# Kernel tuning notes

Measured on AMD Instinct MI355X. Metric: run time of the kernel, lower is better.

Reference implementation:

```python
import jax, jax.numpy as jnp
import numpy as np

EMSIZE = 1024
NHEAD = 16
HEAD = EMSIZE // NHEAD


def setup_inputs() -> dict:
    key = jax.random.key(0)
    ks = jax.random.split(key, 8)
    s = 1.0 / np.sqrt(EMSIZE)
    return {
        "embed": jax.random.normal(ks[0], (2, 2048, EMSIZE), dtype=jnp.float32),
        "q": jax.random.normal(ks[1], (2, 2048, EMSIZE), dtype=jnp.float32),
        "Wk": jax.random.normal(ks[2], (EMSIZE, EMSIZE), dtype=jnp.float32) * s,
        "bk": jnp.zeros((EMSIZE,), dtype=jnp.float32),
        "Wq": jax.random.normal(ks[3], (EMSIZE, EMSIZE), dtype=jnp.float32) * s,
        "bq": jnp.zeros((EMSIZE,), dtype=jnp.float32),
        "Wv": jax.random.normal(ks[4], (EMSIZE, EMSIZE), dtype=jnp.float32) * s,
        "bv": jnp.zeros((EMSIZE,), dtype=jnp.float32),
    }


def _split_heads(x):
    # [b, s, E] -> [b, h, s, d]
    b, s, _ = x.shape
    return x.reshape(b, s, NHEAD, HEAD).transpose(0, 2, 1, 3)


def reference(embed, q, Wk, bk, Wq, bq, Wv, bv):
    # torch Linear: y = x @ W.T + b
    k = _split_heads(embed @ Wk.T + bk)   # [b, h, skv, d]
    qh = _split_heads(q @ Wq.T + bq)      # [b, h, sq, d]
    v = _split_heads(embed @ Wv.T + bv)   # [b, h, skv, d]
    scale = 1.0 / np.sqrt(HEAD).astype(np.float32)
    scores = jnp.einsum("bhqd,bhkd->bhqk", qh, k) * scale
    attn = jax.nn.softmax(scores, axis=-1)  # dropout p=0 -> identity
    ctx = jnp.einsum("bhqk,bhkd->bhqd", attn, v)
    b, h, sq, d = ctx.shape
    return ctx.transpose(0, 2, 1, 3).reshape(b, sq, h * d)
```

## Files before the change

kernel.cpp:

```cpp
#include <hip/hip_runtime.h>
#include <cstdint>
#include <cstddef>


using bf16 = __bf16;
typedef __bf16 bf16x8 __attribute__((ext_vector_type(8)));
typedef float f32x4 __attribute__((ext_vector_type(4)));
typedef float f32x16 __attribute__((ext_vector_type(16)));
using uint32 = unsigned int;

__device__ __forceinline__ void async16(void* lds, const void* g) {
  __builtin_amdgcn_global_load_lds((__attribute__((address_space(1))) void*)g,
                                   (__attribute__((address_space(3))) void*)lds,
                                   16, 0, 0);
}

__device__ __forceinline__ uint32 pack_bf16x2(float lo, float hi_) {
  union { bf16 h[2]; uint32 u; } w;
  w.h[0] = (bf16)lo; w.h[1] = (bf16)hi_;
  return w.u;
}

__global__ void cast_all_kernel(const float* __restrict__ e, const float* __restrict__ q,
                                const float* __restrict__ wk, const float* __restrict__ wq,
                                const float* __restrict__ wv, bf16* __restrict__ dst) {
  int i = blockIdx.x * blockDim.x + threadIdx.x;
  if (i >= 2883584) return;
  const float* src; int off;
  if (i < 1048576)      { src = e;  off = 0; }
  else if (i < 2097152) { src = q;  off = 1048576; }
  else if (i < 2359296) { src = wk; off = 2097152; }
  else if (i < 2621440) { src = wq; off = 2359296; }
  else                  { src = wv; off = 2621440; }
  float4 v = reinterpret_cast<const float4*>(src)[i - off];
  union { bf16 h[4]; unsigned long long u; } o;
  o.h[0] = (bf16)v.x; o.h[1] = (bf16)v.y; o.h[2] = (bf16)v.z; o.h[3] = (bf16)v.w;
  reinterpret_cast<unsigned long long*>(dst)[i] = o.u;
}

__global__ __launch_bounds__(256) void proj_kernel(
    const bf16* __restrict__ emb, const bf16* __restrict__ qin,
    const bf16* __restrict__ wk, const bf16* __restrict__ wq, const bf16* __restrict__ wv,
    const float* __restrict__ bk, const float* __restrict__ bq, const float* __restrict__ bv,
    bf16* __restrict__ Kp, bf16* __restrict__ Qp, bf16* __restrict__ Vt)
{
  __shared__ bf16 As[128 * 64];
  __shared__ bf16 Bs[128 * 64];

  int pid = blockIdx.x;
  int proj = pid >> 8;
  int t = pid & 255;
  int m0 = (t >> 3) * 128;
  int n0 = (t & 7) * 128;

  const bf16* A = (proj == 1) ? qin : emb;
  const bf16* W = (proj == 0) ? wk : (proj == 1) ? wq : wv;
  const float* bias = (proj == 0) ? bk : (proj == 1) ? bq : bv;
  const bool proj2 = (proj == 2);

  int tid = threadIdx.x;
  int lane = tid & 63, wid = tid >> 6;
  int quad = lane >> 4, l16 = lane & 15;
  int moff = (wid & 1) * 64, noff = (wid >> 1) * 64;

  f32x4 zero = {0.f, 0.f, 0.f, 0.f};
  f32x4 acc[4][4];
#pragma unroll
  for (int i = 0; i < 4; i++)
#pragma unroll
    for (int j = 0; j < 4; j++) acc[i][j] = zero;

  for (int kk = 0; kk < 1024; kk += 64) {
    __syncthreads();
#pragma unroll
    for (int i = 0; i < 4; i++) {
      int c = i * 256 + tid;
      int row = c >> 3;
      int ko = ((c ^ row) & 7) << 3;
      async16(&As[(size_t)(i * 256 + wid * 64) * 8], &A[(size_t)(m0 + row) * 1024 + kk + ko]);
      async16(&Bs[(size_t)(i * 256 + wid * 64) * 8], &W[(size_t)(n0 + row) * 1024 + kk + ko]);
    }
    __syncthreads();
#pragma unroll
    for (int ks = 0; ks < 2; ks++) {
      bf16x8 af[4], bfr[4];
#pragma unroll
      for (int i = 0; i < 4; i++) {
        int row = moff + i * 16 + l16;
        af[i] = *reinterpret_cast<const bf16x8*>(&As[row * 64 + ((((ks << 2) | quad) ^ row) & 7) * 8]);
      }
#pragma unroll
      for (int j = 0; j < 4; j++) {
        int row = noff + j * 16 + l16;
        bfr[j] = *reinterpret_cast<const bf16x8*>(&Bs[row * 64 + ((((ks << 2) | quad) ^ row) & 7) * 8]);
      }
      if (proj2) {
#pragma unroll
        for (int i = 0; i < 4; i++)
#pragma unroll
          for (int j = 0; j < 4; j++)
            acc[i][j] = __builtin_amdgcn_mfma_f32_16x16x32_bf16(bfr[j], af[i], acc[i][j], 0, 0, 0);
      } else {
#pragma unroll
        for (int i = 0; i < 4; i++)
#pragma unroll
          for (int j = 0; j < 4; j++)
            acc[i][j] = __builtin_amdgcn_mfma_f32_16x16x32_bf16(af[i], bfr[j], acc[i][j], 0, 0, 0);
      }
    }
  }

  if (proj2) {
#pragma unroll
    for (int i = 0; i < 4; i++) {
      int grow = m0 + moff + i * 16 + l16;
      int bb = grow >> 11;
      int ss = grow & 2047;
#pragma unroll
      for (int j = 0; j < 4; j++) {
#pragma unroll
        for (int r = 0; r < 4; r++) {
          int gcol = n0 + noff + j * 16 + quad * 4 + r;
          int hh = gcol >> 6, dd = gcol & 63;
          int bh = bb * 16 + hh;
          float v = acc[i][j][r] + bias[gcol];
          Vt[((size_t)bh * 64 + dd) * 2048 + ss] = (bf16)v;
        }
      }
    }
  } else {
    float bvv[4];
#pragma unroll
    for (int j = 0; j < 4; j++) bvv[j] = bias[n0 + noff + j * 16 + l16];
    bf16* dst = (proj == 0) ? Kp : Qp;
    const float qs = (proj == 1) ? 0.18033688011112042f : 1.0f;
#pragma unroll
    for (int i = 0; i < 4; i++) {
#pragma unroll
      for (int r = 0; r < 4; r++) {
        int grow = m0 + moff + i * 16 + quad * 4 + r;
        int bb = grow >> 11;
        int ss = grow & 2047;
#pragma unroll
        for (int j = 0; j < 4; j++) {
          int gcol = n0 + noff + j * 16 + l16;
          int hh = gcol >> 6, dd = gcol & 63;
          int bh = bb * 16 + hh;
          float v = (acc[i][j][r] + bvv[j]) * qs;
          dst[((size_t)bh * 2048 + ss) * 64 + dd] = (bf16)v;
        }
      }
    }
  }
}

__global__ __launch_bounds__(256, 4) void attn_kernel(
    const bf16* __restrict__ Qp, const bf16* __restrict__ Kp, const bf16* __restrict__ Vt,
    float* __restrict__ out, float* __restrict__ part1, float* __restrict__ lbuf)
{
  __shared__ bf16 Ks[2][64 * 64];
  __shared__ bf16 Vs[2][64 * 64];

  int bid = blockIdx.x;
  int half = bid & 1;
  int q0 = ((bid >> 1) & 15) << 7;
  int bh = bid >> 5;
  int bb = bh >> 4, hh = bh & 15;
  int g0 = half << 4;

  const bf16* Qg = Qp + (size_t)bh * (2048 * 64);
  const bf16* Kg = Kp + (size_t)bh * (2048 * 64);
  const bf16* Vg = Vt + (size_t)bh * (64 * 2048);

  int tid = threadIdx.x, lane = tid & 63, wid = tid >> 6;
  int l32 = lane & 31;
  int h = lane >> 5;
  int wq0 = q0 + wid * 32;

  auto stage = [&](int kt_, int buf) {
#pragma unroll
    for (int i = 0; i < 2; i++) {
      int c = i * 256 + tid;
      int row = c >> 3;
      int srow = (row & ~12) | ((row & 4) << 1) | ((row & 8) >> 1);
      int ko = ((c ^ row) & 7) << 3;
      async16(&Ks[buf][(size_t)(i * 256 + wid * 64) * 8], &Kg[(size_t)(kt_ * 64 + srow) * 64 + ko]);
      async16(&Vs[buf][(size_t)(i * 256 + wid * 64) * 8], &Vg[(size_t)row * 2048 + kt_ * 64 + ko]);
    }
  };

  bf16x8 qf[4];
#pragma unroll
  for (int s = 0; s < 4; s++)
    qf[s] = *reinterpret_cast<const bf16x8*>(
        &Qg[(size_t)(wq0 + l32) * 64 + s * 16 + h * 8]);

  stage(g0, 0);

  const f32x16 z16 = {0.f, 0.f, 0.f, 0.f, 0.f, 0.f, 0.f, 0.f,
                      0.f, 0.f, 0.f, 0.f, 0.f, 0.f, 0.f, 0.f};
  f32x16 Ov[2];
  Ov[0] = z16; Ov[1] = z16;
  float l_i = 0.f;

  for (int kt = 0; kt < 16; kt++) {
    int cur = kt & 1;
    __syncthreads();
    __builtin_amdgcn_sched_barrier(0);
    if (kt < 15) stage(g0 + kt + 1, cur ^ 1);
    __builtin_amdgcn_sched_barrier(0);

    const bf16* Kc = Ks[cur];
    const bf16* Vc = Vs[cur];

    f32x16 St[2];
#pragma unroll
    for (int t = 0; t < 2; t++) {
      int row = t * 32 + l32;
      {
        bf16x8 kf = *reinterpret_cast<const bf16x8*>(&Kc[row * 64 + ((h ^ row) & 7) * 8]);
        St[t] = __builtin_amdgcn_mfma_f32_32x32x16_bf16(kf, qf[0], z16, 0, 0, 0);
      }
#pragma unroll
      for (int s = 1; s < 4; s++) {
        int j8 = s * 2 + h;
        bf16x8 kf = *reinterpret_cast<const bf16x8*>(&Kc[row * 64 + ((j8 ^ row) & 7) * 8]);
        St[t] = __builtin_amdgcn_mfma_f32_32x32x16_bf16(kf, qf[s], St[t], 0, 0, 0);
      }
    }

#pragma unroll
    for (int t = 0; t < 2; t++)
#pragma unroll
      for (int i = 0; i < 16; i++) {
        float p = __builtin_amdgcn_exp2f(St[t][i]);
        St[t][i] = p;
        l_i += p;
      }

#pragma unroll
    for (int t = 0; t < 2; t++)
#pragma unroll
      for (int g = 0; g < 2; g++) {
        union { uint32 u[4]; bf16x8 v; } pb;
#pragma unroll
        for (int i = 0; i < 4; i++)
          pb.u[i] = pack_bf16x2(St[t][g * 8 + 2 * i], St[t][g * 8 + 2 * i + 1]);
        int j8 = t * 4 + g * 2 + h;
#pragma unroll
        for (int dt = 0; dt < 2; dt++) {
          int rowv = dt * 32 + l32;
          bf16x8 vf = *reinterpret_cast<const bf16x8*>(&Vc[rowv * 64 + ((j8 ^ rowv) & 7) * 8]);
          Ov[dt] = __builtin_amdgcn_mfma_f32_32x32x16_bf16(vf, pb.v, Ov[dt], 0, 0, 0);
        }
      }
  }

  float l_tot = l_i + __shfl_xor(l_i, 32);
  int q = wq0 + l32;
  float* dstO = (half == 0 ? out : part1) + ((size_t)bb * 2048 + q) * 1024 + hh * 64;
#pragma unroll
  for (int dt = 0; dt < 2; dt++)
#pragma unroll
    for (int g = 0; g < 4; g++) {
      float4 o;
      o.x = Ov[dt][4 * g + 0];
      o.y = Ov[dt][4 * g + 1];
      o.z = Ov[dt][4 * g + 2];
      o.w = Ov[dt][4 * g + 3];
      *reinterpret_cast<float4*>(&dstO[dt * 32 + g * 8 + 4 * h]) = o;
    }
  if (h == 0) lbuf[half * 65536 + (bh << 11) + q] = l_tot;
}

__global__ __launch_bounds__(256) void combine_kernel(
    float* __restrict__ out, const float* __restrict__ part1,
    const float* __restrict__ lbuf) {
  int i = blockIdx.x * 256 + threadIdx.x;
  int e = i << 2;
  int brow = e >> 10;
  int b = brow >> 11;
  int hcol = (e >> 6) & 15;
  int srow = brow & 2047;
  int lidx = ((b * 16 + hcol) << 11) + srow;
  float inv = 1.0f / (lbuf[lidx] + lbuf[65536 + lidx]);
  float4 a = reinterpret_cast<const float4*>(out)[i];
  float4 p = reinterpret_cast<const float4*>(part1)[i];
  float4 r;
  r.x = (a.x + p.x) * inv;
  r.y = (a.y + p.y) * inv;
  r.z = (a.z + p.z) * inv;
  r.w = (a.w + p.w) * inv;
  reinterpret_cast<float4*>(out)[i] = r;
}

extern "C" void kernel_launch(void* const* d_in, const int* in_sizes, int n_in,
                              void* d_out, int out_size, void* d_ws, size_t ws_size,
                              hipStream_t stream) {
  (void)in_sizes; (void)n_in; (void)out_size; (void)ws_size;
  const float* embed = (const float*)d_in[0];
  const float* qin   = (const float*)d_in[1];
  const float* Wk    = (const float*)d_in[2];
  const float* bk    = (const float*)d_in[3];
  const float* Wq    = (const float*)d_in[4];
  const float* bq    = (const float*)d_in[5];
  const float* Wv    = (const float*)d_in[6];
  const float* bv    = (const float*)d_in[7];
  float* out = (float*)d_out;

  bf16* ws = (bf16*)d_ws;
  bf16* emb_bf = ws;
  bf16* q_bf   = emb_bf + 4194304;
  bf16* wk_bf  = q_bf   + 4194304;
  bf16* wq_bf  = wk_bf  + 1048576;
  bf16* wv_bf  = wq_bf  + 1048576;
  bf16* Kp     = wv_bf  + 1048576;
  bf16* Qp     = Kp     + 4194304;
  bf16* Vt     = Qp     + 4194304;

  float* part1 = (float*)d_ws;
  float* lbuf  = part1 + 4194304;

  cast_all_kernel<<<11264, 256, 0, stream>>>(embed, qin, Wk, Wq, Wv, ws);

  proj_kernel<<<768, 256, 0, stream>>>(emb_bf, q_bf, wk_bf, wq_bf, wv_bf,
                                       bk, bq, bv, Kp, Qp, Vt);
  attn_kernel<<<1024, 256, 0, stream>>>(Qp, Kp, Vt, out, part1, lbuf);
  combine_kernel<<<4096, 256, 0, stream>>>(out, part1, lbuf);
}
```

Before: 194.5 us.

## Generalize attention KV split to four ways when workspace allows

```diff
diff --git a/kernel.cpp b/kernel.cpp
--- a/kernel.cpp
+++ b/kernel.cpp
@@ -154,19 +154,22 @@
   }
 }
 
-__global__ __launch_bounds__(256, 4) void attn_kernel(
+__global__ __launch_bounds__(256, 5) void attn_kernel(
     const bf16* __restrict__ Qp, const bf16* __restrict__ Kp, const bf16* __restrict__ Vt,
-    float* __restrict__ out, float* __restrict__ part1, float* __restrict__ lbuf)
+    float* __restrict__ out, float* __restrict__ part, float* __restrict__ lbuf,
+    int lsplit)
 {
   __shared__ bf16 Ks[2][64 * 64];
   __shared__ bf16 Vs[2][64 * 64];
 
   int bid = blockIdx.x;
-  int half = bid & 1;
-  int q0 = ((bid >> 1) & 15) << 7;
-  int bh = bid >> 5;
+  int nsplit = 1 << lsplit;
+  int half = bid & (nsplit - 1);
+  int q0 = ((bid >> lsplit) & 15) << 7;
+  int bh = bid >> (4 + lsplit);
   int bb = bh >> 4, hh = bh & 15;
-  int g0 = half << 4;
+  int ntiles = 32 >> lsplit;
+  int g0 = half * ntiles;
 
   const bf16* Qg = Qp + (size_t)bh * (2048 * 64);
   const bf16* Kg = Kp + (size_t)bh * (2048 * 64);
@@ -203,11 +206,11 @@
   Ov[0] = z16; Ov[1] = z16;
   float l_i = 0.f;
 
-  for (int kt = 0; kt < 16; kt++) {
+  for (int kt = 0; kt < ntiles; kt++) {
     int cur = kt & 1;
     __syncthreads();
     __builtin_amdgcn_sched_barrier(0);
-    if (kt < 15) stage(g0 + kt + 1, cur ^ 1);
+    if (kt < ntiles - 1) stage(g0 + kt + 1, cur ^ 1);
     __builtin_amdgcn_sched_barrier(0);
 
     const bf16* Kc = Ks[cur];
@@ -258,7 +261,8 @@
 
   float l_tot = l_i + __shfl_xor(l_i, 32);
   int q = wq0 + l32;
-  float* dstO = (half == 0 ? out : part1) + ((size_t)bb * 2048 + q) * 1024 + hh * 64;
+  float* dstO = (half == 0 ? out : part + (size_t)(half - 1) * 4194304)
+                + ((size_t)bb * 2048 + q) * 1024 + hh * 64;
 #pragma unroll
   for (int dt = 0; dt < 2; dt++)
 #pragma unroll
@@ -274,8 +278,8 @@
 }
 
 __global__ __launch_bounds__(256) void combine_kernel(
-    float* __restrict__ out, const float* __restrict__ part1,
-    const float* __restrict__ lbuf) {
+    float* __restrict__ out, const float* __restrict__ part,
+    const float* __restrict__ lbuf, int nsplit) {
   int i = blockIdx.x * 256 + threadIdx.x;
   int e = i << 2;
   int brow = e >> 10;
@@ -283,21 +287,24 @@
   int hcol = (e >> 6) & 15;
   int srow = brow & 2047;
   int lidx = ((b * 16 + hcol) << 11) + srow;
-  float inv = 1.0f / (lbuf[lidx] + lbuf[65536 + lidx]);
+  float lsum = lbuf[lidx];
+#pragma unroll 3
+  for (int s = 1; s < nsplit; s++) lsum += lbuf[s * 65536 + lidx];
   float4 a = reinterpret_cast<const float4*>(out)[i];
-  float4 p = reinterpret_cast<const float4*>(part1)[i];
-  float4 r;
-  r.x = (a.x + p.x) * inv;
-  r.y = (a.y + p.y) * inv;
-  r.z = (a.z + p.z) * inv;
-  r.w = (a.w + p.w) * inv;
-  reinterpret_cast<float4*>(out)[i] = r;
+#pragma unroll 3
+  for (int s = 1; s < nsplit; s++) {
+    float4 p = reinterpret_cast<const float4*>(part)[(size_t)(s - 1) * 1048576 + i];
+    a.x += p.x; a.y += p.y; a.z += p.z; a.w += p.w;
+  }
+  float inv = 1.0f / lsum;
+  a.x *= inv; a.y *= inv; a.z *= inv; a.w *= inv;
+  reinterpret_cast<float4*>(out)[i] = a;
 }
 
 extern "C" void kernel_launch(void* const* d_in, const int* in_sizes, int n_in,
                               void* d_out, int out_size, void* d_ws, size_t ws_size,
                               hipStream_t stream) {
-  (void)in_sizes; (void)n_in; (void)out_size; (void)ws_size;
+  (void)in_sizes; (void)n_in; (void)out_size;
   const float* embed = (const float*)d_in[0];
   const float* qin   = (const float*)d_in[1];
   const float* Wk    = (const float*)d_in[2];
@@ -318,13 +325,21 @@
   bf16* Qp     = Kp     + 4194304;
   bf16* Vt     = Qp     + 4194304;
 
-  float* part1 = (float*)d_ws;
-  float* lbuf  = part1 + 4194304;
+  const bool big = (ws_size >= 99614720ull);
+  const int lsplit = big ? 2 : 1;
+  float* part, *lbuf;
+  if (big) {
+    part = (float*)((char*)d_ws + 48234496);
+    lbuf = part + 3 * 4194304;
+  } else {
+    part = (float*)d_ws;
+    lbuf = part + 4194304;
+  }
 
   cast_all_kernel<<<11264, 256, 0, stream>>>(embed, qin, Wk, Wq, Wv, ws);
 
   proj_kernel<<<768, 256, 0, stream>>>(emb_bf, q_bf, wk_bf, wq_bf, wv_bf,
                                        bk, bq, bv, Kp, Qp, Vt);
-  attn_kernel<<<1024, 256, 0, stream>>>(Qp, Kp, Vt, out, part1, lbuf);
-  combine_kernel<<<4096, 256, 0, stream>>>(out, part1, lbuf);
-}
+  attn_kernel<<<512 << lsplit, 256, 0, stream>>>(Qp, Kp, Vt, out, part, lbuf, lsplit);
+  combine_kernel<<<4096, 256, 0, stream>>>(out, part, lbuf, 1 << lsplit);
+}
```

Result: slower. 227.5 us (+17.0%).
